# Performance work log

Measured on AMD Instinct MI355X. Metric: run time of the kernel, lower is better.

## Reference

```python
import jax, jax.numpy as jnp
import numpy as np
from jax import lax


def binarize_weight(w):
    # per-output-channel scaling alpha = mean(|w|), binary weight = sign(w)*alpha
    alpha = jnp.mean(jnp.abs(w), axis=(1, 2, 3), keepdims=True)  # [O,1,1,1]
    wb = jnp.sign(w) * alpha
    # STE: forward uses wb, gradient passes straight through to w
    return w + lax.stop_gradient(wb - w)


def pixel_unshuffle2(x):
    # NCHW, factor 2: out[:, c*4 + i*2 + j] = x[:, c, i::2, j::2]
    B, C, H, W = x.shape
    x = x.reshape(B, C, H // 2, 2, W // 2, 2)
    x = x.transpose(0, 1, 3, 5, 2, 4)
    return x.reshape(B, C * 4, H // 2, W // 2)


def setup_inputs() -> dict:
    key = jax.random.key(0)
    ks = jax.random.split(key, 5)
    x = jax.random.normal(ks[0], (16, 256, 128, 128), dtype=jnp.float32)
    conv_w = jax.random.normal(ks[1], (128, 256, 3, 3), dtype=jnp.float32) * 0.05
    move1_b = jax.random.normal(ks[2], (128,), dtype=jnp.float32) * 0.01
    prelu_w = jax.random.uniform(ks[3], (128,), dtype=jnp.float32) * 0.25
    move2_b = jax.random.normal(ks[4], (128,), dtype=jnp.float32) * 0.01
    scale = jnp.ones((1,), dtype=jnp.float32)
    return {"x": x, "conv_w": conv_w, "move1_b": move1_b,
            "prelu_w": prelu_w, "move2_b": move2_b, "scale": scale}


def reference(x, conv_w, move1_b, prelu_w, move2_b, scale):
    wb = binarize_weight(conv_w)
    out = lax.conv_general_dilated(
        x, wb, window_strides=(1, 1), padding=((1, 1), (1, 1)),
        dimension_numbers=("NCHW", "OIHW", "NCHW"))  # [B,128,H,W]
    out = out + move1_b[None, :, None, None]
    a = prelu_w[None, :, None, None]
    out = jnp.where(out > 0, out, a * out)
    out = out + move2_b[None, :, None, None]
    shortcut = x[:, : x.shape[1] // 2, :, :] * scale[0]
    out = out + shortcut
    return pixel_unshuffle2(out)  # [B,512,H/2,W/2]
```

## Files before the change

kernel.cpp:

```cpp
#include <hip/hip_runtime.h>
#include <stdint.h>

typedef unsigned short ushort_t;
typedef __bf16 bf16x8 __attribute__((ext_vector_type(8)));
typedef float f32x4 __attribute__((ext_vector_type(4)));

#define NB   16
#define CIN  256
#define COUT 128
#define HH   128
#define WW   128
#define HP   130
#define WP   130
#define KTAP 9
#define KTOT 2304

__device__ __forceinline__ ushort_t f2bf(float f) {
  union { float f; uint32_t u; } v; v.f = f;
  uint32_t u = v.u;
  uint32_t r = (u + 0x7fffu + ((u >> 16) & 1u)) >> 16;
  return (ushort_t)r;
}
__device__ __forceinline__ float bf2f(ushort_t b) {
  union { uint32_t u; float f; } v; v.u = ((uint32_t)b) << 16;
  return v.f;
}
__device__ __forceinline__ void gload_lds16(const void* g, void* l) {
  __builtin_amdgcn_global_load_lds((const __attribute__((address_space(1))) void*)g,
                                   (__attribute__((address_space(3))) void*)l, 16, 0, 0);
}

__global__ void prep_w_kernel(const float* __restrict__ w,
                              ushort_t* __restrict__ sgnW,
                              float* __restrict__ alpha) {
  int o = blockIdx.x, c = threadIdx.x;
  const float* wo = w + (size_t)o * KTOT + c * 9;
  float s = 0.f;
#pragma unroll
  for (int tap = 0; tap < 9; ++tap) {
    float v = wo[tap];
    s += fabsf(v);
    ushort_t sg = (v > 0.f) ? 0x3F80 : (v < 0.f ? 0xBF80 : 0);
    sgnW[((size_t)tap * COUT + o) * CIN + c] = sg;
  }
  __shared__ float red[4];
  for (int off = 32; off; off >>= 1) s += __shfl_down(s, off, 64);
  if (!(c & 63)) red[c >> 6] = s;
  __syncthreads();
  if (!c) alpha[o] = (red[0] + red[1] + red[2] + red[3]) * (1.f / (float)KTOT);
}

__global__ void pad_kernel(ushort_t* __restrict__ xT) {
  int blk = blockIdx.x;
  int b = blk / 130, h = blk - b * 130;
  int t = threadIdx.x;
  uint32_t* row = (uint32_t*)(xT + ((size_t)b * HP + h) * WP * CIN);
  if (h == 0 || h == 129) {
    for (int i = t; i < WP * CIN / 2; i += 256) row[i] = 0;
  } else {
    if (t < 128) row[t] = 0;
    else         row[129 * (CIN / 2) + (t - 128)] = 0;
  }
}

__global__ void transpose_kernel(const float* __restrict__ x,
                                 ushort_t* __restrict__ xT) {
  int bid = blockIdx.x;
  int ct = bid & 3;
  int wt = (bid >> 2) & 1;
  int h  = (bid >> 3) & 127;
  int b  = bid >> 10;
  int c0 = ct * 64, w0 = wt * 64;
  __shared__ float tile[64][65];
  int t = threadIdx.x;
  const float* src = x + (((size_t)b * CIN + c0) * HH + h) * WW + w0;
#pragma unroll 4
  for (int it = 0; it < 16; ++it) {
    int cl = it * 4 + (t >> 6);
    tile[cl][t & 63] = src[(size_t)cl * (HH * WW) + (t & 63)];
  }
  __syncthreads();
  int cb = (t & 7) * 8;
  int wl = t >> 3;
#pragma unroll
  for (int wp = 0; wp < 2; ++wp) {
    int w = wp * 32 + wl;
    uint32_t pk[4];
#pragma unroll
    for (int j = 0; j < 4; ++j)
      pk[j] = (uint32_t)f2bf(tile[cb + 2 * j][w]) |
              ((uint32_t)f2bf(tile[cb + 2 * j + 1][w]) << 16);
    size_t idx = ((((size_t)b * HP + h + 1) * WP) + (w0 + w + 1)) * CIN + c0 + cb;
    *(uint4*)(xT + idx) = *(uint4*)pk;
  }
}

__global__ __launch_bounds__(256, 4) void conv_gemm(
    const ushort_t* __restrict__ xT, const ushort_t* __restrict__ sgnW,
    const float* __restrict__ alpha, const float* __restrict__ mv1,
    const float* __restrict__ pw, const float* __restrict__ mv2,
    const float* __restrict__ scale, float* __restrict__ out) {
  __shared__ __align__(16) ushort_t As[128 * 64];
  __shared__ __align__(16) ushort_t Bs[128 * 64];

  int bid = blockIdx.x;
  int wg = ((bid & 7) << 8) | (bid >> 3);
  int b = wg >> 7, h = wg & 127;

  int t = threadIdx.x, wv = t >> 6, l = t & 63;
  int wr = wv >> 1, wc = wv & 1;

  int crow = l >> 3;
  int se = (l & 7) ^ crow;
  int lg = l >> 4, rA = l & 15;

  f32x4 acc[4][4] = {};

  const ushort_t* xb = xT + ((size_t)b * HP + h) * WP * CIN;

  for (int i0q = 0; i0q < 4; ++i0q) {
#pragma unroll
    for (int tap = 0; tap < 9; ++tap) {
      const int kh = tap / 3, kw = tap - kh * 3;
      __syncthreads();
      const ushort_t* gA = xb + (kh * WP + kw) * CIN + (i0q << 6) + se * 8;
      const ushort_t* gB = sgnW + (size_t)tap * (COUT * CIN) + (i0q << 6) + se * 8;
#pragma unroll
      for (int q = 0; q < 4; ++q) {
        int c = wv * 4 + q;
        int m = c * 8 + crow;
        gload_lds16(gA + (size_t)m * CIN, (char*)As + c * 1024);
        gload_lds16(gB + (size_t)m * CIN, (char*)Bs + c * 1024);
      }
      __syncthreads();
#pragma unroll
      for (int kk = 0; kk < 2; ++kk) {
        bf16x8 av[4], bv[4];
#pragma unroll
        for (int mi = 0; mi < 4; ++mi) {
          int m = wr * 64 + mi * 16 + rA;
          int slot = (kk * 4 + lg) ^ (m & 7);
          av[mi] = *(const bf16x8*)((const char*)As + m * 128 + slot * 16);
        }
#pragma unroll
        for (int ni = 0; ni < 4; ++ni) {
          int o = wc * 64 + ni * 16 + rA;
          int slot = (kk * 4 + lg) ^ (o & 7);
          bv[ni] = *(const bf16x8*)((const char*)Bs + o * 128 + slot * 16);
        }
#pragma unroll
        for (int mi = 0; mi < 4; ++mi)
#pragma unroll
          for (int ni = 0; ni < 4; ++ni)
            acc[mi][ni] = __builtin_amdgcn_mfma_f32_16x16x32_bf16(av[mi], bv[ni], acc[mi][ni], 0, 0, 0);
      }
    }
  }

  float sc0 = scale[0];
  const ushort_t* scrow = xT + (((size_t)b * HP + h + 1) * WP + 1) * CIN;
  size_t outBase = (((size_t)b * 512 + (h & 1) * 2) * 64 + (h >> 1)) * 64;
#pragma unroll
  for (int ni = 0; ni < 4; ++ni) {
    int o = wc * 64 + ni * 16 + rA;
    float al = alpha[o], b1 = mv1[o], p = pw[o], b2 = mv2[o];
#pragma unroll
    for (int mi = 0; mi < 4; ++mi) {
#pragma unroll
      for (int r = 0; r < 4; ++r) {
        int w = wr * 64 + mi * 16 + lg * 4 + r;
        float v = acc[mi][ni][r] * al + b1;
        v = v > 0.f ? v : p * v;
        v += b2;
        v += bf2f(scrow[(size_t)w * CIN + o]) * sc0;
        out[outBase + (size_t)(o * 4 + (w & 1)) * 4096 + (w >> 1)] = v;
      }
    }
  }
}

extern "C" void kernel_launch(void* const* d_in, const int* in_sizes, int n_in,
                              void* d_out, int out_size, void* d_ws, size_t ws_size,
                              hipStream_t stream) {
  const float* x      = (const float*)d_in[0];
  const float* conv_w = (const float*)d_in[1];
  const float* mv1    = (const float*)d_in[2];
  const float* pw     = (const float*)d_in[3];
  const float* mv2    = (const float*)d_in[4];
  const float* scale  = (const float*)d_in[5];
  float* out = (float*)d_out;

  const size_t XT_ELEMS = (size_t)NB * HP * WP * CIN;
  ushort_t* xT   = (ushort_t*)d_ws;
  ushort_t* sgnW = xT + XT_ELEMS;
  float*    alpha = (float*)(sgnW + (size_t)KTAP * COUT * CIN);

  prep_w_kernel<<<COUT, 256, 0, stream>>>(conv_w, sgnW, alpha);
  pad_kernel<<<NB * HP, 256, 0, stream>>>(xT);
  transpose_kernel<<<NB * HH * 2 * 4, 256, 0, stream>>>(x, xT);
  conv_gemm<<<NB * HH, 256, 0, stream>>>(xT, sgnW, alpha, mv1, pw, mv2, scale, out);
}
```

Before: 679.8 us.

## Enlarge conv GEMM tile to two output rows and stage epilogue through LDS

Each workgroup now handles two output rows (M=256) with 512 threads, so each loaded weight tile is reused across twice as many pixels and the B-operand traffic per output is halved. The epilogue stages results through an XOR-swizzled LDS buffer in four chunks, so the pixel-unshuffled output is written with coalesced 64-float rows instead of strided scattered stores. The cost is larger LDS use (48KB), extra barriers in the epilogue, and possibly lower occupancy with 512-thread blocks.

```diff
diff --git a/kernel.cpp b/kernel.cpp
--- a/kernel.cpp
+++ b/kernel.cpp
@@ -95,17 +95,20 @@
   }
 }
 
-__global__ __launch_bounds__(256, 4) void conv_gemm(
+__global__ __launch_bounds__(512, 4) void conv_gemm(
     const ushort_t* __restrict__ xT, const ushort_t* __restrict__ sgnW,
     const float* __restrict__ alpha, const float* __restrict__ mv1,
     const float* __restrict__ pw, const float* __restrict__ mv2,
     const float* __restrict__ scale, float* __restrict__ out) {
-  __shared__ __align__(16) ushort_t As[128 * 64];
-  __shared__ __align__(16) ushort_t Bs[128 * 64];
+  __shared__ __align__(16) char smem[49152];
+  ushort_t* As = (ushort_t*)smem;
+  ushort_t* Bs = (ushort_t*)(smem + 32768);
+  float*    ep = (float*)smem;
 
   int bid = blockIdx.x;
-  int wg = ((bid & 7) << 8) | (bid >> 3);
-  int b = wg >> 7, h = wg & 127;
+  int wg = ((bid & 7) << 7) | (bid >> 3);
+  int b = wg >> 6, hp = wg & 63;
+  int h = hp << 1;
 
   int t = threadIdx.x, wv = t >> 6, l = t & 63;
   int wr = wv >> 1, wc = wv & 1;
@@ -119,18 +122,25 @@
   const ushort_t* xb = xT + ((size_t)b * HP + h) * WP * CIN;
 
   for (int i0q = 0; i0q < 4; ++i0q) {
+    int i0 = i0q << 6;
 #pragma unroll
     for (int tap = 0; tap < 9; ++tap) {
       const int kh = tap / 3, kw = tap - kh * 3;
       __syncthreads();
-      const ushort_t* gA = xb + (kh * WP + kw) * CIN + (i0q << 6) + se * 8;
-      const ushort_t* gB = sgnW + (size_t)tap * (COUT * CIN) + (i0q << 6) + se * 8;
 #pragma unroll
       for (int q = 0; q < 4; ++q) {
-        int c = wv * 4 + q;
-        int m = c * 8 + crow;
-        gload_lds16(gA + (size_t)m * CIN, (char*)As + c * 1024);
-        gload_lds16(gB + (size_t)m * CIN, (char*)Bs + c * 1024);
+        int ca = wv * 4 + q;
+        int m = ca * 8 + crow;
+        int hh = m >> 7, w = m & 127;
+        gload_lds16(xb + ((size_t)(hh + kh) * WP + w + kw) * CIN + i0 + se * 8,
+                    (char*)As + ca * 1024);
+      }
+#pragma unroll
+      for (int q = 0; q < 2; ++q) {
+        int cb = wv * 2 + q;
+        int o = cb * 8 + crow;
+        gload_lds16(sgnW + ((size_t)tap * COUT + o) * CIN + i0 + se * 8,
+                    (char*)Bs + cb * 1024);
       }
       __syncthreads();
 #pragma unroll
@@ -158,23 +168,44 @@
   }
 
   float sc0 = scale[0];
-  const ushort_t* scrow = xT + (((size_t)b * HP + h + 1) * WP + 1) * CIN;
-  size_t outBase = (((size_t)b * 512 + (h & 1) * 2) * 64 + (h >> 1)) * 64;
-#pragma unroll
-  for (int ni = 0; ni < 4; ++ni) {
-    int o = wc * 64 + ni * 16 + rA;
-    float al = alpha[o], b1 = mv1[o], p = pw[o], b2 = mv2[o];
-#pragma unroll
-    for (int mi = 0; mi < 4; ++mi) {
-#pragma unroll
-      for (int r = 0; r < 4; ++r) {
-        int w = wr * 64 + mi * 16 + lg * 4 + r;
-        float v = acc[mi][ni][r] * al + b1;
-        v = v > 0.f ? v : p * v;
-        v += b2;
-        v += bf2f(scrow[(size_t)w * CIN + o]) * sc0;
-        out[outBase + (size_t)(o * 4 + (w & 1)) * 4096 + (w >> 1)] = v;
-      }
+  int hh0 = wr >> 1;
+  const ushort_t* scrow = xT + (((size_t)b * HP + h + hh0 + 1) * WP + 1) * CIN;
+  int myChunk = hh0 * 2 + wc;
+
+  for (int ch = 0; ch < 4; ++ch) {
+    __syncthreads();
+    if (myChunk == ch) {
+#pragma unroll
+      for (int ni = 0; ni < 4; ++ni) {
+        int o = wc * 64 + ni * 16 + rA;
+        float al = alpha[o], b1 = mv1[o], p = pw[o], b2 = mv2[o];
+#pragma unroll
+        for (int mi = 0; mi < 4; ++mi) {
+#pragma unroll
+          for (int r = 0; r < 4; ++r) {
+            int m = wr * 64 + mi * 16 + lg * 4 + r;
+            int w = m & 127;
+            float v = acc[mi][ni][r] * al + b1;
+            v = v > 0.f ? v : p * v;
+            v += b2;
+            v += bf2f(scrow[(size_t)w * CIN + o]) * sc0;
+            int slot = (ni * 16 + rA) * 2 + (w & 1);
+            int ww2 = w >> 1;
+            ep[slot * 64 + (ww2 ^ (slot & 31))] = v;
+          }
+        }
+      }
+    }
+    __syncthreads();
+    int hh = ch >> 1, c = ch & 1;
+#pragma unroll
+    for (int j = 0; j < 16; ++j) {
+      int idx = j * 512 + t;
+      int ww2 = idx & 63, slot = idx >> 6;
+      float v = ep[slot * 64 + (ww2 ^ (slot & 31))];
+      int o = c * 64 + (slot >> 1);
+      int oc4 = o * 4 + hh * 2 + (slot & 1);
+      out[(((size_t)b * 512 + oc4) * 64 + hp) * 64 + ww2] = v;
     }
   }
 }
@@ -198,5 +229,5 @@
   prep_w_kernel<<<COUT, 256, 0, stream>>>(conv_w, sgnW, alpha);
   pad_kernel<<<NB * HP, 256, 0, stream>>>(xT);
   transpose_kernel<<<NB * HH * 2 * 4, 256, 0, stream>>>(x, xT);
-  conv_gemm<<<NB * HH, 256, 0, stream>>>(xT, sgnW, alpha, mv1, pw, mv2, scale, out);
-}
+  conv_gemm<<<NB * HH / 2, 512, 0, stream>>>(xT, sgnW, alpha, mv1, pw, mv2, scale, out);
+}
```

Result: slower. 1.007 ms (+48.2%).

## Drop LDS staging; load pre-swizzled MFMA fragments directly from global memory

Applied to the files above, without the earlier changes.

Binarized weights are written in an MFMA-fragment-ordered layout so each lane reads its B operand with one contiguous 16-byte load. The conv GEMM no longer stages A and B through shared memory with barriers. Each wave instead loads its activation rows and all 128 output-channel fragments straight from global/L2, with a 32x128 tile per wave. This removes LDS traffic and __syncthreads, but each wave now re-reads the full weight tile from cache and uses more registers, so launch bounds drop to 3 blocks per SIMD.

```diff
diff --git a/kernel.cpp b/kernel.cpp
--- a/kernel.cpp
+++ b/kernel.cpp
@@ -12,7 +12,6 @@
 #define WW   128
 #define HP   130
 #define WP   130
-#define KTAP 9
 #define KTOT 2304
 
 __device__ __forceinline__ ushort_t f2bf(float f) {
@@ -25,23 +24,24 @@
   union { uint32_t u; float f; } v; v.u = ((uint32_t)b) << 16;
   return v.f;
 }
-__device__ __forceinline__ void gload_lds16(const void* g, void* l) {
-  __builtin_amdgcn_global_load_lds((const __attribute__((address_space(1))) void*)g,
-                                   (__attribute__((address_space(3))) void*)l, 16, 0, 0);
-}
 
 __global__ void prep_w_kernel(const float* __restrict__ w,
-                              ushort_t* __restrict__ sgnW,
+                              ushort_t* __restrict__ pk,
                               float* __restrict__ alpha) {
   int o = blockIdx.x, c = threadIdx.x;
   const float* wo = w + (size_t)o * KTOT + c * 9;
+  int ni = o >> 4, rA = o & 15;
+  int i0q = c >> 6, r6 = c & 63;
+  int kk = r6 >> 5, r5 = r6 & 31, lg = r5 >> 3, j = r5 & 7;
+  int l = lg * 16 + rA;
   float s = 0.f;
 #pragma unroll
   for (int tap = 0; tap < 9; ++tap) {
     float v = wo[tap];
     s += fabsf(v);
     ushort_t sg = (v > 0.f) ? 0x3F80 : (v < 0.f ? 0xBF80 : 0);
-    sgnW[((size_t)tap * COUT + o) * CIN + c] = sg;
+    size_t f = ((((size_t)(i0q * 9 + tap) * 2 + kk) * 8 + ni) * 64 + l) * 8 + j;
+    pk[f] = sg;
   }
   __shared__ float red[4];
   for (int off = 32; off; off >>= 1) s += __shfl_down(s, off, 64);
@@ -85,74 +85,58 @@
 #pragma unroll
   for (int wp = 0; wp < 2; ++wp) {
     int w = wp * 32 + wl;
-    uint32_t pk[4];
+    uint32_t pkd[4];
 #pragma unroll
     for (int j = 0; j < 4; ++j)
-      pk[j] = (uint32_t)f2bf(tile[cb + 2 * j][w]) |
-              ((uint32_t)f2bf(tile[cb + 2 * j + 1][w]) << 16);
+      pkd[j] = (uint32_t)f2bf(tile[cb + 2 * j][w]) |
+               ((uint32_t)f2bf(tile[cb + 2 * j + 1][w]) << 16);
     size_t idx = ((((size_t)b * HP + h + 1) * WP) + (w0 + w + 1)) * CIN + c0 + cb;
-    *(uint4*)(xT + idx) = *(uint4*)pk;
+    *(uint4*)(xT + idx) = *(uint4*)pkd;
   }
 }
 
-__global__ __launch_bounds__(256, 4) void conv_gemm(
-    const ushort_t* __restrict__ xT, const ushort_t* __restrict__ sgnW,
+__global__ __launch_bounds__(256, 3) void conv_gemm(
+    const ushort_t* __restrict__ xT, const ushort_t* __restrict__ pk,
     const float* __restrict__ alpha, const float* __restrict__ mv1,
     const float* __restrict__ pw, const float* __restrict__ mv2,
     const float* __restrict__ scale, float* __restrict__ out) {
-  __shared__ __align__(16) ushort_t As[128 * 64];
-  __shared__ __align__(16) ushort_t Bs[128 * 64];
-
   int bid = blockIdx.x;
   int wg = ((bid & 7) << 8) | (bid >> 3);
   int b = wg >> 7, h = wg & 127;
 
   int t = threadIdx.x, wv = t >> 6, l = t & 63;
-  int wr = wv >> 1, wc = wv & 1;
-
-  int crow = l >> 3;
-  int se = (l & 7) ^ crow;
   int lg = l >> 4, rA = l & 15;
 
-  f32x4 acc[4][4] = {};
+  f32x4 acc[2][8] = {};
 
-  const ushort_t* xb = xT + ((size_t)b * HP + h) * WP * CIN;
+  const ushort_t* xb = xT + ((size_t)b * HP + h) * WP * CIN
+                          + ((size_t)(wv * 32 + rA)) * CIN + lg * 8;
+  const ushort_t* pB = pk + l * 8;
 
   for (int i0q = 0; i0q < 4; ++i0q) {
+    int i0 = i0q << 6;
+    const size_t bq = (size_t)i0q * 9 * 2 * 8 * 512;
 #pragma unroll
-    for (int tap = 0; tap < 9; ++tap) {
-      const int kh = tap / 3, kw = tap - kh * 3;
-      __syncthreads();
-      const ushort_t* gA = xb + (kh * WP + kw) * CIN + (i0q << 6) + se * 8;
-      const ushort_t* gB = sgnW + (size_t)tap * (COUT * CIN) + (i0q << 6) + se * 8;
+    for (int kh = 0; kh < 3; ++kh) {
 #pragma unroll
-      for (int q = 0; q < 4; ++q) {
-        int c = wv * 4 + q;
-        int m = c * 8 + crow;
-        gload_lds16(gA + (size_t)m * CIN, (char*)As + c * 1024);
-        gload_lds16(gB + (size_t)m * CIN, (char*)Bs + c * 1024);
-      }
-      __syncthreads();
+      for (int kw = 0; kw < 3; ++kw) {
+        const int tap = kh * 3 + kw;
+        const ushort_t* pA = xb + (kh * WP + kw) * CIN + i0;
+        const ushort_t* pT = pB + bq + (size_t)tap * 2 * 8 * 512;
 #pragma unroll
-      for (int kk = 0; kk < 2; ++kk) {
-        bf16x8 av[4], bv[4];
+        for (int kk = 0; kk < 2; ++kk) {
+          bf16x8 a0 = *(const bf16x8*)(pA + kk * 32);
+          bf16x8 a1 = *(const bf16x8*)(pA + 4096 + kk * 32);
+          bf16x8 bv[8];
 #pragma unroll
-        for (int mi = 0; mi < 4; ++mi) {
-          int m = wr * 64 + mi * 16 + rA;
-          int slot = (kk * 4 + lg) ^ (m & 7);
-          av[mi] = *(const bf16x8*)((const char*)As + m * 128 + slot * 16);
+          for (int ni = 0; ni < 8; ++ni)
+            bv[ni] = *(const bf16x8*)(pT + (size_t)(kk * 8 + ni) * 512);
+#pragma unroll
+          for (int ni = 0; ni < 8; ++ni) {
+            acc[0][ni] = __builtin_amdgcn_mfma_f32_16x16x32_bf16(a0, bv[ni], acc[0][ni], 0, 0, 0);
+            acc[1][ni] = __builtin_amdgcn_mfma_f32_16x16x32_bf16(a1, bv[ni], acc[1][ni], 0, 0, 0);
+          }
         }
-#pragma unroll
-        for (int ni = 0; ni < 4; ++ni) {
-          int o = wc * 64 + ni * 16 + rA;
-          int slot = (kk * 4 + lg) ^ (o & 7);
-          bv[ni] = *(const bf16x8*)((const char*)Bs + o * 128 + slot * 16);
-        }
-#pragma unroll
-        for (int mi = 0; mi < 4; ++mi)
-#pragma unroll
-          for (int ni = 0; ni < 4; ++ni)
-            acc[mi][ni] = __builtin_amdgcn_mfma_f32_16x16x32_bf16(av[mi], bv[ni], acc[mi][ni], 0, 0, 0);
       }
     }
   }
@@ -161,14 +145,14 @@
   const ushort_t* scrow = xT + (((size_t)b * HP + h + 1) * WP + 1) * CIN;
   size_t outBase = (((size_t)b * 512 + (h & 1) * 2) * 64 + (h >> 1)) * 64;
 #pragma unroll
-  for (int ni = 0; ni < 4; ++ni) {
-    int o = wc * 64 + ni * 16 + rA;
+  for (int ni = 0; ni < 8; ++ni) {
+    int o = ni * 16 + rA;
     float al = alpha[o], b1 = mv1[o], p = pw[o], b2 = mv2[o];
 #pragma unroll
-    for (int mi = 0; mi < 4; ++mi) {
+    for (int mi = 0; mi < 2; ++mi) {
 #pragma unroll
       for (int r = 0; r < 4; ++r) {
-        int w = wr * 64 + mi * 16 + lg * 4 + r;
+        int w = wv * 32 + mi * 16 + lg * 4 + r;
         float v = acc[mi][ni][r] * al + b1;
         v = v > 0.f ? v : p * v;
         v += b2;
@@ -191,12 +175,13 @@
   float* out = (float*)d_out;
 
   const size_t XT_ELEMS = (size_t)NB * HP * WP * CIN;
+  const size_t PK_ELEMS = (size_t)4 * 9 * 2 * 8 * 64 * 8;
   ushort_t* xT   = (ushort_t*)d_ws;
-  ushort_t* sgnW = xT + XT_ELEMS;
-  float*    alpha = (float*)(sgnW + (size_t)KTAP * COUT * CIN);
+  ushort_t* pk   = xT + XT_ELEMS;
+  float*    alpha = (float*)(pk + PK_ELEMS);
 
-  prep_w_kernel<<<COUT, 256, 0, stream>>>(conv_w, sgnW, alpha);
+  prep_w_kernel<<<COUT, 256, 0, stream>>>(conv_w, pk, alpha);
   pad_kernel<<<NB * HP, 256, 0, stream>>>(xT);
   transpose_kernel<<<NB * HH * 2 * 4, 256, 0, stream>>>(x, xT);
-  conv_gemm<<<NB * HH, 256, 0, stream>>>(xT, sgnW, alpha, mv1, pw, mv2, scale, out);
+  conv_gemm<<<NB * HH, 256, 0, stream>>>(xT, pk, alpha, mv1, pw, mv2, scale, out);
 }
```

After: 779.3 us. 1.15x slower.
